# Kernel optimization log

Measured on AMD Instinct MI355X. Metric: run time of the kernel, lower is better.

Reference implementation:

```python
import jax, jax.numpy as jnp
import numpy as np

B, T, QD, KD, E, H, L = 4, 512, 256, 256, 256, 8, 4
DH = E // H
SHAPES = np.array([[64, 64], [32, 32], [16, 16], [8, 8]], dtype=np.int64)
S = int(np.sum(SHAPES[:, 0] * SHAPES[:, 1]))  # 5440


def setup_inputs() -> dict:
    key = jax.random.key(0)
    ks = jax.random.split(key, 16)
    std = 0.02
    return {
        "q": jax.random.normal(ks[0], (B, T, QD), jnp.float32),
        "k": jax.random.normal(ks[1], (B, S, KD), jnp.float32),
        "v": jax.random.normal(ks[2], (B, S, KD), jnp.float32),
        "Wq": jax.random.normal(ks[3], (E, QD), jnp.float32) * std,
        "bq": jnp.zeros((E,), jnp.float32),
        "Wk": jax.random.normal(ks[4], (E, KD), jnp.float32) * std,
        "bk": jnp.zeros((E,), jnp.float32),
        "Wv": jax.random.normal(ks[5], (E, KD), jnp.float32) * std,
        "bv": jnp.zeros((E,), jnp.float32),
        "Wo": jax.random.normal(ks[6], (QD, E), jnp.float32) * std,
        "bo": jnp.zeros((QD,), jnp.float32),
        "Wl": jax.random.normal(ks[7], (H * L, QD), jnp.float32) * std,
        "bl": jnp.zeros((H * L,), jnp.float32),
        "k_spatial_shapes": SHAPES,  # static int metadata (split sizes)
    }


def _heads(x, b):
    # [b, s, E] -> [b, H, s, DH]
    return x.reshape(b, -1, H, DH).transpose(0, 2, 1, 3)


def reference(q, k, v, Wq, bq, Wk, bk, Wv, bv, Wo, bo, Wl, bl, k_spatial_shapes):
    scale = DH ** -0.5
    bsz = q.shape[0]
    # per-head, per-level gate: [B, H, T, L], softmax over levels
    gates = jax.nn.softmax(
        (q @ Wl.T + bl).reshape(bsz, -1, H, L).transpose(0, 2, 1, 3), axis=-1
    )
    qs = _heads((q @ Wq.T + bq) * scale, bsz)   # [B,H,T,DH]
    ks_ = _heads(k @ Wk.T + bk, bsz)            # [B,H,S,DH]
    vs = _heads(v @ Wv.T + bv, bsz)             # [B,H,S,DH]
    scores = jnp.einsum("bhtd,bhsd->bhts", qs, ks_)  # [B,H,T,S]
    sizes = [int(h_ * w_) for h_, w_ in np.asarray(k_spatial_shapes)]
    offs = np.concatenate([[0], np.cumsum(sizes)])
    # segmented softmax per level, weighted by the learned level gate
    pieces = [
        jax.nn.softmax(scores[..., offs[i]:offs[i + 1]], axis=-1) * gates[..., i:i + 1]
        for i in range(len(sizes))
    ]
    attn = jnp.concatenate(pieces, axis=-1)  # [B,H,T,S]
    out = jnp.einsum("bhts,bhsd->bhtd", attn, vs)
    out = out.transpose(0, 2, 1, 3).reshape(bsz, -1, E)
    out = out @ Wo.T + bo
    return out, attn
```

## Files before the change

### kernel.cpp

```cpp
#include <hip/hip_runtime.h>
#include <hip/hip_bf16.h>

#define Bn 4
#define Hn 8
#define Tn 512
#define Sn 5440
#define DHn 32
#define En 256

typedef short bf16x8 __attribute__((ext_vector_type(8)));
typedef float f32x4 __attribute__((ext_vector_type(4)));

static __device__ __forceinline__ unsigned short f2bf(float f) {
    union { float f; unsigned u; } c; c.f = f;
    unsigned r = c.u + 0x7fffu + ((c.u >> 16) & 1u);
    return (unsigned short)(r >> 16);
}

static __device__ __forceinline__ unsigned int cvtpk(float a, float b) {
    __hip_bfloat162 h = __float22bfloat162_rn(make_float2(a, b));
    unsigned int u; __builtin_memcpy(&u, &h, 4); return u;
}

__global__ __launch_bounds__(256) void gates_kernel(
// ... 136 lines not shown
    }
}

__global__ __launch_bounds__(256) void proj_out(
    const float* __restrict__ A, const float* __restrict__ W,
    const float* __restrict__ bias, float* __restrict__ out)
{
    __shared__ unsigned short As[128][40];
    __shared__ unsigned short Ws[128][40];

    int tid = threadIdx.x;
    int l = tid & 63, wid = tid >> 6;
    int wr = wid >> 1, wc = wid & 1;
    int lr = l & 15, lg = l >> 4;
    int row0 = blockIdx.x * 128, col0 = blockIdx.y * 128;

    f32x4 acc[4][4] = {};
    gemm_core(A, W, row0, col0, tid, wr, wc, lr, lg, As, Ws, acc);

    #pragma unroll
    for (int i = 0; i < 4; i++) {
        int m0 = row0 + wr*64 + i*16 + lg*4;
        #pragma unroll
        for (int j = 0; j < 4; j++) {
            int col = col0 + wc*64 + j*16 + lr;
            float bvv = bias[col];
            #pragma unroll
            for (int r = 0; r < 4; r++)
                __builtin_nontemporal_store(acc[i][j][r] + bvv, &out[(size_t)(m0 + r)*256 + col]);
        }
    }
}

__global__ __launch_bounds__(256) void attn_fused(
    const unsigned short* __restrict__ qs, const unsigned short* __restrict__ ks,
    const unsigned short* __restrict__ vt, const float* __restrict__ gates,
    float* __restrict__ attn_out, float* __restrict__ o_tmp)
{
    __shared__ char plds[4][2048];
    __shared__ float lsum[4][4][16];
    __shared__ float denom[4][16];
    __shared__ float outred[4][16][32];

    int n = blockIdx.x;
    int bh = ((n >> 8) << 3) | (n & 7);
    int tt = (n >> 3) & 31;
    int t0 = tt << 4;
    int b = bh >> 3, h = bh & 7;
    int tid = threadIdx.x;
    int l = tid & 63, w = tid >> 6;
    int lr = l & 15, lg = l >> 4;

    bf16x8 aq = *(const bf16x8*)(qs + ((size_t)bh*Tn + t0 + lr)*DHn + lg*8);
    const unsigned short* kb = ks + (size_t)bh * Sn * DHn;
    const unsigned short* vb = vt + (size_t)bh * DHn * Sn;
    const f32x4 fzero = {0.f, 0.f, 0.f, 0.f};

    float lp0 = 0.f, lp1 = 0.f, lp2 = 0.f, lp3 = 0.f;
    bf16x8 kf0, kf1, kf2, kf3;
    {
        const unsigned short* kc_ = kb + (size_t)w * 64 * DHn;
        kf0 = *(const bf16x8*)(kc_ + (size_t)(lr     )*DHn + lg*8);
        kf1 = *(const bf16x8*)(kc_ + (size_t)(16 + lr)*DHn + lg*8);
        kf2 = *(const bf16x8*)(kc_ + (size_t)(32 + lr)*DHn + lg*8);
        kf3 = *(const bf16x8*)(kc_ + (size_t)(48 + lr)*DHn + lg*8);
    }
    for (int c = w; c < 85; c += 4) {
        bf16x8 kn0, kn1, kn2, kn3;
        int cn = c + 4;
        if (cn < 85) {
            const unsigned short* kc_ = kb + (size_t)cn * 64 * DHn;
            kn0 = *(const bf16x8*)(kc_ + (size_t)(lr     )*DHn + lg*8);
            kn1 = *(const bf16x8*)(kc_ + (size_t)(16 + lr)*DHn + lg*8);
            kn2 = *(const bf16x8*)(kc_ + (size_t)(32 + lr)*DHn + lg*8);
            kn3 = *(const bf16x8*)(kc_ + (size_t)(48 + lr)*DHn + lg*8);
        }
        __builtin_amdgcn_s_setprio(1);
        f32x4 s0 = __builtin_amdgcn_mfma_f32_16x16x32_bf16(kf0, aq, fzero, 0, 0, 0);
        f32x4 s1 = __builtin_amdgcn_mfma_f32_16x16x32_bf16(kf1, aq, fzero, 0, 0, 0);
        f32x4 s2 = __builtin_amdgcn_mfma_f32_16x16x32_bf16(kf2, aq, fzero, 0, 0, 0);
        f32x4 s3 = __builtin_amdgcn_mfma_f32_16x16x32_bf16(kf3, aq, fzero, 0, 0, 0);
        __builtin_amdgcn_s_setprio(0);
        float es = exp2f(s0[0]) + exp2f(s0[1]) + exp2f(s0[2]) + exp2f(s0[3])
                 + exp2f(s1[0]) + exp2f(s1[1]) + exp2f(s1[2]) + exp2f(s1[3])
                 + exp2f(s2[0]) + exp2f(s2[1]) + exp2f(s2[2]) + exp2f(s2[3])
                 + exp2f(s3[0]) + exp2f(s3[1]) + exp2f(s3[2]) + exp2f(s3[3]);
        if      (c < 64) lp0 += es;
        else if (c < 80) lp1 += es;
        else if (c < 84) lp2 += es;
        else             lp3 += es;
        kf0 = kn0; kf1 = kn1; kf2 = kn2; kf3 = kn3;
    }
    {
        float v;
        v = lp0; v += __shfl_xor(v, 16); v += __shfl_xor(v, 32); lp0 = v;
        v = lp1; v += __shfl_xor(v, 16); v += __shfl_xor(v, 32); lp1 = v;
        v = lp2; v += __shfl_xor(v, 16); v += __shfl_xor(v, 32); lp2 = v;
        v = lp3; v += __shfl_xor(v, 16); v += __shfl_xor(v, 32); lp3 = v;
    }
    if (l < 16) {
        lsum[w][0][lr] = lp0; lsum[w][1][lr] = lp1;
        lsum[w][2][lr] = lp2; lsum[w][3][lr] = lp3;
    }
    __syncthreads();
    if (tid < 64) {
        int seg = tid >> 4, row = tid & 15;
        denom[seg][row] = lsum[0][seg][row] + lsum[1][seg][row] + lsum[2][seg][row] + lsum[3][seg][row];
    }
    __syncthreads();

    float cf0, cf1, cf2, cf3;
    {
        const float* g = gates + ((size_t)bh*Tn + t0 + lr)*4;
        cf0 = g[0] / denom[0][lr];
        cf1 = g[1] / denom[1][lr];
        cf2 = g[2] / denom[2][lr];
        cf3 = g[3] / denom[3][lr];
    }

    f32x4 acc0 = fzero, acc1 = fzero;
    char* pbase = plds[w];
    float* arow = attn_out + ((size_t)bh*Tn + t0 + lr)*Sn;
    int swz = (lr & 7) << 4;

    bf16x8 vf0, vf1, vf2, vf3;
    {
        const unsigned short* kc_ = kb + (size_t)w * 64 * DHn;
        kf0 = *(const bf16x8*)(kc_ + (size_t)(lr     )*DHn + lg*8);
        kf1 = *(const bf16x8*)(kc_ + (size_t)(16 + lr)*DHn + lg*8);
        kf2 = *(const bf16x8*)(kc_ + (size_t)(32 + lr)*DHn + lg*8);
        kf3 = *(const bf16x8*)(kc_ + (size_t)(48 + lr)*DHn + lg*8);
        vf0 = *(const bf16x8*)(vb + (size_t)(lr     )*Sn + w*64      + lg*8);
        vf1 = *(const bf16x8*)(vb + (size_t)(16 + lr)*Sn + w*64      + lg*8);
        vf2 = *(const bf16x8*)(vb + (size_t)(lr     )*Sn + w*64 + 32 + lg*8);
        vf3 = *(const bf16x8*)(vb + (size_t)(16 + lr)*Sn + w*64 + 32 + lg*8);
    }

    for (int c = w; c < 85; c += 4) {
        bf16x8 kn0, kn1, kn2, kn3, vn0, vn1, vn2, vn3;
        int cn = c + 4;
        if (cn < 85) {
            const unsigned short* kc_ = kb + (size_t)cn * 64 * DHn;
            kn0 = *(const bf16x8*)(kc_ + (size_t)(lr     )*DHn + lg*8);
            kn1 = *(const bf16x8*)(kc_ + (size_t)(16 + lr)*DHn + lg*8);
            kn2 = *(const bf16x8*)(kc_ + (size_t)(32 + lr)*DHn + lg*8);
            kn3 = *(const bf16x8*)(kc_ + (size_t)(48 + lr)*DHn + lg*8);
            vn0 = *(const bf16x8*)(vb + (size_t)(lr     )*Sn + cn*64      + lg*8);
            vn1 = *(const bf16x8*)(vb + (size_t)(16 + lr)*Sn + cn*64      + lg*8);
            vn2 = *(const bf16x8*)(vb + (size_t)(lr     )*Sn + cn*64 + 32 + lg*8);
            vn3 = *(const bf16x8*)(vb + (size_t)(16 + lr)*Sn + cn*64 + 32 + lg*8);
        }
        float cf = (c < 64) ? cf0 : (c < 80) ? cf1 : (c < 84) ? cf2 : cf3;

        __builtin_amdgcn_s_setprio(1);
        f32x4 s0 = __builtin_amdgcn_mfma_f32_16x16x32_bf16(kf0, aq, fzero, 0, 0, 0);
        f32x4 s1 = __builtin_amdgcn_mfma_f32_16x16x32_bf16(kf1, aq, fzero, 0, 0, 0);
        f32x4 s2 = __builtin_amdgcn_mfma_f32_16x16x32_bf16(kf2, aq, fzero, 0, 0, 0);
        f32x4 s3 = __builtin_amdgcn_mfma_f32_16x16x32_bf16(kf3, aq, fzero, 0, 0, 0);
        __builtin_amdgcn_s_setprio(0);

        {
            f32x4 av;
            av[0] = exp2f(s0[0])*cf; av[1] = exp2f(s0[1])*cf; av[2] = exp2f(s0[2])*cf; av[3] = exp2f(s0[3])*cf;
            __builtin_nontemporal_store(av, (f32x4*)(arow + c*64 +   0 + 4*lg));
            uint2 pk; pk.x = cvtpk(av[0], av[1]); pk.y = cvtpk(av[2], av[3]);
            *(uint2*)(pbase + ((lr*128 +   0 + lg*8) ^ swz)) = pk;
            av[0] = exp2f(s1[0])*cf; av[1] = exp2f(s1[1])*cf; av[2] = exp2f(s1[2])*cf; av[3] = exp2f(s1[3])*cf;
            __builtin_nontemporal_store(av, (f32x4*)(arow + c*64 +  16 + 4*lg));
            pk.x = cvtpk(av[0], av[1]); pk.y = cvtpk(av[2], av[3]);
            *(uint2*)(pbase + ((lr*128 +  32 + lg*8) ^ swz)) = pk;
            av[0] = exp2f(s2[0])*cf; av[1] = exp2f(s2[1])*cf; av[2] = exp2f(s2[2])*cf; av[3] = exp2f(s2[3])*cf;
            __builtin_nontemporal_store(av, (f32x4*)(arow + c*64 +  32 + 4*lg));
            pk.x = cvtpk(av[0], av[1]); pk.y = cvtpk(av[2], av[3]);
            *(uint2*)(pbase + ((lr*128 +  64 + lg*8) ^ swz)) = pk;
            av[0] = exp2f(s3[0])*cf; av[1] = exp2f(s3[1])*cf; av[2] = exp2f(s3[2])*cf; av[3] = exp2f(s3[3])*cf;
            __builtin_nontemporal_store(av, (f32x4*)(arow + c*64 +  48 + 4*lg));
            pk.x = cvtpk(av[0], av[1]); pk.y = cvtpk(av[2], av[3]);
            *(uint2*)(pbase + ((lr*128 +  96 + lg*8) ^ swz)) = pk;
        }

        __builtin_amdgcn_s_setprio(1);
        {
            bf16x8 pa0 = *(const bf16x8*)(pbase + ((lr*128 +      lg*16) ^ swz));
            acc0 = __builtin_amdgcn_mfma_f32_16x16x32_bf16(pa0, vf0, acc0, 0, 0, 0);
            acc1 = __builtin_amdgcn_mfma_f32_16x16x32_bf16(pa0, vf1, acc1, 0, 0, 0);
            bf16x8 pa1 = *(const bf16x8*)(pbase + ((lr*128 + 64 + lg*16) ^ swz));
            acc0 = __builtin_amdgcn_mfma_f32_16x16x32_bf16(pa1, vf2, acc0, 0, 0, 0);
            acc1 = __builtin_amdgcn_mfma_f32_16x16x32_bf16(pa1, vf3, acc1, 0, 0, 0);
        }
        __builtin_amdgcn_s_setprio(0);

        kf0 = kn0; kf1 = kn1; kf2 = kn2; kf3 = kn3;
        vf0 = vn0; vf1 = vn1; vf2 = vn2; vf3 = vn3;
    }

    #pragma unroll
    for (int r = 0; r < 4; r++) {
        outred[w][4*lg + r][lr]      = acc0[r];
        outred[w][4*lg + r][16 + lr] = acc1[r];
    }
    __syncthreads();
    #pragma unroll
    for (int i = 0; i < 2; i++) {
        int idx = tid + i*256;
        int row = idx >> 5, d = idx & 31;
        float sum = outred[0][row][d] + outred[1][row][d] + outred[2][row][d] + outred[3][row][d];
        __builtin_nontemporal_store(sum, &o_tmp[((size_t)(b*Tn + t0 + row))*En + h*DHn + d]);
    }
}

extern "C" void kernel_launch(void* const* d_in, const int* in_sizes, int n_in,
                              void* d_out, int out_size, void* d_ws, size_t ws_size,
                              hipStream_t stream)
{
    const float* q  = (const float*)d_in[0];
    const float* k  = (const float*)d_in[1];
    const float* v  = (const float*)d_in[2];
    const float* Wq = (const float*)d_in[3];
    const float* bq = (const float*)d_in[4];
    const float* Wk = (const float*)d_in[5];
    const float* bk = (const float*)d_in[6];
    const float* Wv = (const float*)d_in[7];
    const float* bv = (const float*)d_in[8];
    const float* Wo = (const float*)d_in[9];
    const float* bo = (const float*)d_in[10];
    const float* Wl = (const float*)d_in[11];
    const float* bl = (const float*)d_in[12];

    float* out  = (float*)d_out;
    float* attn = out + (size_t)Bn*Tn*256;

    char* ws = (char*)d_ws;
    unsigned short* qs    = (unsigned short*)ws;
    unsigned short* ksb   = (unsigned short*)(ws + (1u<<20));
    unsigned short* vtb   = (unsigned short*)(ws + (1u<<20) + 11141120u);
    float*          gates = (float*)(ws + (1u<<20) + 2u*11141120u);
    float*          o_tmp = (float*)(ws + (1u<<20) + 2u*11141120u + 262144u);

    gates_kernel<<<Bn*Tn/8, 256, 0, stream>>>(q, Wl, bl, gates);
    proj_kvq<<<dim3((Bn*Sn)/128, 2, 3), 256, 0, stream>>>(
        k, Wk, bk, v, Wv, bv, q, Wq, bq, ksb, vtb, qs);
    attn_fused<<<Bn*Hn*(Tn/16), 256, 0, stream>>>(qs, ksb, vtb, gates, attn, o_tmp);
    proj_out<<<dim3((Bn*Tn)/128, 2), 256, 0, stream>>>(o_tmp, Wo, bo, out);
}
```

Before: 182.7 us.

## Split attention into unnormalized PV pass and separate attn-store kernel

The attention kernel now does one pass over K/V. It accumulates unnormalized exp-weighted V products into four per-level accumulators and applies gate/denominator scaling only at the end, which removes the second QK/PV sweep. Writing the large attn probability matrix moves to a new kernel that recomputes QK scores from the denominators stored in workspace. This trades the duplicated PV work and the serialization of stores behind the reductions for an extra launch, a recomputed QK, and dropped software prefetching. Without max subtraction, keeping unnormalized sums in bf16 P carries some precision risk.

```diff
diff --git a/kernel.cpp b/kernel.cpp
--- a/kernel.cpp
+++ b/kernel.cpp
@@ -192,14 +192,14 @@
     }
 }
 
-__global__ __launch_bounds__(256) void attn_fused(
+__global__ __launch_bounds__(256) void attn_pv(
     const unsigned short* __restrict__ qs, const unsigned short* __restrict__ ks,
     const unsigned short* __restrict__ vt, const float* __restrict__ gates,
-    float* __restrict__ attn_out, float* __restrict__ o_tmp)
+    float* __restrict__ denom_g, float* __restrict__ o_tmp)
 {
     __shared__ char plds[4][2048];
     __shared__ float lsum[4][4][16];
-    __shared__ float denom[4][16];
+    __shared__ float denomS[4][16];
     __shared__ float outred[4][16][32];
 
     int n = blockIdx.x;
@@ -217,40 +217,78 @@
     const f32x4 fzero = {0.f, 0.f, 0.f, 0.f};
 
     float lp0 = 0.f, lp1 = 0.f, lp2 = 0.f, lp3 = 0.f;
-    bf16x8 kf0, kf1, kf2, kf3;
-    {
-        const unsigned short* kc_ = kb + (size_t)w * 64 * DHn;
-        kf0 = *(const bf16x8*)(kc_ + (size_t)(lr     )*DHn + lg*8);
-        kf1 = *(const bf16x8*)(kc_ + (size_t)(16 + lr)*DHn + lg*8);
-        kf2 = *(const bf16x8*)(kc_ + (size_t)(32 + lr)*DHn + lg*8);
-        kf3 = *(const bf16x8*)(kc_ + (size_t)(48 + lr)*DHn + lg*8);
-    }
+    f32x4 A0a = fzero, A0b = fzero, A1a = fzero, A1b = fzero;
+    f32x4 A2a = fzero, A2b = fzero, A3a = fzero, A3b = fzero;
+
+    char* pbase = plds[w];
+    int swz = (lr & 7) << 4;
+
     for (int c = w; c < 85; c += 4) {
-        bf16x8 kn0, kn1, kn2, kn3;
-        int cn = c + 4;
-        if (cn < 85) {
-            const unsigned short* kc_ = kb + (size_t)cn * 64 * DHn;
-            kn0 = *(const bf16x8*)(kc_ + (size_t)(lr     )*DHn + lg*8);
-            kn1 = *(const bf16x8*)(kc_ + (size_t)(16 + lr)*DHn + lg*8);
-            kn2 = *(const bf16x8*)(kc_ + (size_t)(32 + lr)*DHn + lg*8);
-            kn3 = *(const bf16x8*)(kc_ + (size_t)(48 + lr)*DHn + lg*8);
-        }
-        __builtin_amdgcn_s_setprio(1);
+        const unsigned short* kc_ = kb + (size_t)c * 64 * DHn;
+        bf16x8 kf0 = *(const bf16x8*)(kc_ + (size_t)(lr     )*DHn + lg*8);
+        bf16x8 kf1 = *(const bf16x8*)(kc_ + (size_t)(16 + lr)*DHn + lg*8);
+        bf16x8 kf2 = *(const bf16x8*)(kc_ + (size_t)(32 + lr)*DHn + lg*8);
+        bf16x8 kf3 = *(const bf16x8*)(kc_ + (size_t)(48 + lr)*DHn + lg*8);
+
         f32x4 s0 = __builtin_amdgcn_mfma_f32_16x16x32_bf16(kf0, aq, fzero, 0, 0, 0);
         f32x4 s1 = __builtin_amdgcn_mfma_f32_16x16x32_bf16(kf1, aq, fzero, 0, 0, 0);
         f32x4 s2 = __builtin_amdgcn_mfma_f32_16x16x32_bf16(kf2, aq, fzero, 0, 0, 0);
         f32x4 s3 = __builtin_amdgcn_mfma_f32_16x16x32_bf16(kf3, aq, fzero, 0, 0, 0);
-        __builtin_amdgcn_s_setprio(0);
-        float es = exp2f(s0[0]) + exp2f(s0[1]) + exp2f(s0[2]) + exp2f(s0[3])
-                 + exp2f(s1[0]) + exp2f(s1[1]) + exp2f(s1[2]) + exp2f(s1[3])
-                 + exp2f(s2[0]) + exp2f(s2[1]) + exp2f(s2[2]) + exp2f(s2[3])
-                 + exp2f(s3[0]) + exp2f(s3[1]) + exp2f(s3[2]) + exp2f(s3[3]);
-        if      (c < 64) lp0 += es;
-        else if (c < 80) lp1 += es;
-        else if (c < 84) lp2 += es;
-        else             lp3 += es;
-        kf0 = kn0; kf1 = kn1; kf2 = kn2; kf3 = kn3;
-    }
+
+        float es;
+        {
+            float e0 = exp2f(s0[0]), e1 = exp2f(s0[1]), e2 = exp2f(s0[2]), e3 = exp2f(s0[3]);
+            uint2 pk; pk.x = cvtpk(e0, e1); pk.y = cvtpk(e2, e3);
+            *(uint2*)(pbase + ((lr*128 +   0 + lg*8) ^ swz)) = pk;
+            es = e0 + e1 + e2 + e3;
+            e0 = exp2f(s1[0]); e1 = exp2f(s1[1]); e2 = exp2f(s1[2]); e3 = exp2f(s1[3]);
+            pk.x = cvtpk(e0, e1); pk.y = cvtpk(e2, e3);
+            *(uint2*)(pbase + ((lr*128 +  32 + lg*8) ^ swz)) = pk;
+            es += e0 + e1 + e2 + e3;
+            e0 = exp2f(s2[0]); e1 = exp2f(s2[1]); e2 = exp2f(s2[2]); e3 = exp2f(s2[3]);
+            pk.x = cvtpk(e0, e1); pk.y = cvtpk(e2, e3);
+            *(uint2*)(pbase + ((lr*128 +  64 + lg*8) ^ swz)) = pk;
+            es += e0 + e1 + e2 + e3;
+            e0 = exp2f(s3[0]); e1 = exp2f(s3[1]); e2 = exp2f(s3[2]); e3 = exp2f(s3[3]);
+            pk.x = cvtpk(e0, e1); pk.y = cvtpk(e2, e3);
+            *(uint2*)(pbase + ((lr*128 +  96 + lg*8) ^ swz)) = pk;
+            es += e0 + e1 + e2 + e3;
+        }
+
+        bf16x8 vf0 = *(const bf16x8*)(vb + (size_t)(lr     )*Sn + c*64      + lg*8);
+        bf16x8 vf1 = *(const bf16x8*)(vb + (size_t)(16 + lr)*Sn + c*64      + lg*8);
+        bf16x8 vf2 = *(const bf16x8*)(vb + (size_t)(lr     )*Sn + c*64 + 32 + lg*8);
+        bf16x8 vf3 = *(const bf16x8*)(vb + (size_t)(16 + lr)*Sn + c*64 + 32 + lg*8);
+        bf16x8 pa0 = *(const bf16x8*)(pbase + ((lr*128 +      lg*16) ^ swz));
+        bf16x8 pa1 = *(const bf16x8*)(pbase + ((lr*128 + 64 + lg*16) ^ swz));
+
+        if (c < 64) {
+            lp0 += es;
+            A0a = __builtin_amdgcn_mfma_f32_16x16x32_bf16(pa0, vf0, A0a, 0, 0, 0);
+            A0b = __builtin_amdgcn_mfma_f32_16x16x32_bf16(pa0, vf1, A0b, 0, 0, 0);
+            A0a = __builtin_amdgcn_mfma_f32_16x16x32_bf16(pa1, vf2, A0a, 0, 0, 0);
+            A0b = __builtin_amdgcn_mfma_f32_16x16x32_bf16(pa1, vf3, A0b, 0, 0, 0);
+        } else if (c < 80) {
+            lp1 += es;
+            A1a = __builtin_amdgcn_mfma_f32_16x16x32_bf16(pa0, vf0, A1a, 0, 0, 0);
+            A1b = __builtin_amdgcn_mfma_f32_16x16x32_bf16(pa0, vf1, A1b, 0, 0, 0);
+            A1a = __builtin_amdgcn_mfma_f32_16x16x32_bf16(pa1, vf2, A1a, 0, 0, 0);
+            A1b = __builtin_amdgcn_mfma_f32_16x16x32_bf16(pa1, vf3, A1b, 0, 0, 0);
+        } else if (c < 84) {
+            lp2 += es;
+            A2a = __builtin_amdgcn_mfma_f32_16x16x32_bf16(pa0, vf0, A2a, 0, 0, 0);
+            A2b = __builtin_amdgcn_mfma_f32_16x16x32_bf16(pa0, vf1, A2b, 0, 0, 0);
+            A2a = __builtin_amdgcn_mfma_f32_16x16x32_bf16(pa1, vf2, A2a, 0, 0, 0);
+            A2b = __builtin_amdgcn_mfma_f32_16x16x32_bf16(pa1, vf3, A2b, 0, 0, 0);
+        } else {
+            lp3 += es;
+            A3a = __builtin_amdgcn_mfma_f32_16x16x32_bf16(pa0, vf0, A3a, 0, 0, 0);
+            A3b = __builtin_amdgcn_mfma_f32_16x16x32_bf16(pa0, vf1, A3b, 0, 0, 0);
+            A3a = __builtin_amdgcn_mfma_f32_16x16x32_bf16(pa1, vf2, A3a, 0, 0, 0);
+            A3b = __builtin_amdgcn_mfma_f32_16x16x32_bf16(pa1, vf3, A3b, 0, 0, 0);
+        }
+    }
+
     {
         float v;
         v = lp0; v += __shfl_xor(v, 16); v += __shfl_xor(v, 32); lp0 = v;
@@ -265,99 +303,22 @@
     __syncthreads();
     if (tid < 64) {
         int seg = tid >> 4, row = tid & 15;
-        denom[seg][row] = lsum[0][seg][row] + lsum[1][seg][row] + lsum[2][seg][row] + lsum[3][seg][row];
+        float d = lsum[0][seg][row] + lsum[1][seg][row] + lsum[2][seg][row] + lsum[3][seg][row];
+        denomS[seg][row] = d;
+        denom_g[((size_t)bh*Tn + t0 + row)*4 + seg] = d;
     }
     __syncthreads();
-
-    float cf0, cf1, cf2, cf3;
-    {
-        const float* g = gates + ((size_t)bh*Tn + t0 + lr)*4;
-        cf0 = g[0] / denom[0][lr];
-        cf1 = g[1] / denom[1][lr];
-        cf2 = g[2] / denom[2][lr];
-        cf3 = g[3] / denom[3][lr];
-    }
-
-    f32x4 acc0 = fzero, acc1 = fzero;
-    char* pbase = plds[w];
-    float* arow = attn_out + ((size_t)bh*Tn + t0 + lr)*Sn;
-    int swz = (lr & 7) << 4;
-
-    bf16x8 vf0, vf1, vf2, vf3;
-    {
-        const unsigned short* kc_ = kb + (size_t)w * 64 * DHn;
-        kf0 = *(const bf16x8*)(kc_ + (size_t)(lr     )*DHn + lg*8);
-        kf1 = *(const bf16x8*)(kc_ + (size_t)(16 + lr)*DHn + lg*8);
-        kf2 = *(const bf16x8*)(kc_ + (size_t)(32 + lr)*DHn + lg*8);
-        kf3 = *(const bf16x8*)(kc_ + (size_t)(48 + lr)*DHn + lg*8);
-        vf0 = *(const bf16x8*)(vb + (size_t)(lr     )*Sn + w*64      + lg*8);
-        vf1 = *(const bf16x8*)(vb + (size_t)(16 + lr)*Sn + w*64      + lg*8);
-        vf2 = *(const bf16x8*)(vb + (size_t)(lr     )*Sn + w*64 + 32 + lg*8);
-        vf3 = *(const bf16x8*)(vb + (size_t)(16 + lr)*Sn + w*64 + 32 + lg*8);
-    }
-
-    for (int c = w; c < 85; c += 4) {
-        bf16x8 kn0, kn1, kn2, kn3, vn0, vn1, vn2, vn3;
-        int cn = c + 4;
-        if (cn < 85) {
-            const unsigned short* kc_ = kb + (size_t)cn * 64 * DHn;
-            kn0 = *(const bf16x8*)(kc_ + (size_t)(lr     )*DHn + lg*8);
-            kn1 = *(const bf16x8*)(kc_ + (size_t)(16 + lr)*DHn + lg*8);
-            kn2 = *(const bf16x8*)(kc_ + (size_t)(32 + lr)*DHn + lg*8);
-            kn3 = *(const bf16x8*)(kc_ + (size_t)(48 + lr)*DHn + lg*8);
-            vn0 = *(const bf16x8*)(vb + (size_t)(lr     )*Sn + cn*64      + lg*8);
-            vn1 = *(const bf16x8*)(vb + (size_t)(16 + lr)*Sn + cn*64      + lg*8);
-            vn2 = *(const bf16x8*)(vb + (size_t)(lr     )*Sn + cn*64 + 32 + lg*8);
-            vn3 = *(const bf16x8*)(vb + (size_t)(16 + lr)*Sn + cn*64 + 32 + lg*8);
-        }
-        float cf = (c < 64) ? cf0 : (c < 80) ? cf1 : (c < 84) ? cf2 : cf3;
-
-        __builtin_amdgcn_s_setprio(1);
-        f32x4 s0 = __builtin_amdgcn_mfma_f32_16x16x32_bf16(kf0, aq, fzero, 0, 0, 0);
-        f32x4 s1 = __builtin_amdgcn_mfma_f32_16x16x32_bf16(kf1, aq, fzero, 0, 0, 0);
-        f32x4 s2 = __builtin_amdgcn_mfma_f32_16x16x32_bf16(kf2, aq, fzero, 0, 0, 0);
-        f32x4 s3 = __builtin_amdgcn_mfma_f32_16x16x32_bf16(kf3, aq, fzero, 0, 0, 0);
-        __builtin_amdgcn_s_setprio(0);
-
-        {
-            f32x4 av;
-            av[0] = exp2f(s0[0])*cf; av[1] = exp2f(s0[1])*cf; av[2] = exp2f(s0[2])*cf; av[3] = exp2f(s0[3])*cf;
-            __builtin_nontemporal_store(av, (f32x4*)(arow + c*64 +   0 + 4*lg));
-            uint2 pk; pk.x = cvtpk(av[0], av[1]); pk.y = cvtpk(av[2], av[3]);
-            *(uint2*)(pbase + ((lr*128 +   0 + lg*8) ^ swz)) = pk;
-            av[0] = exp2f(s1[0])*cf; av[1] = exp2f(s1[1])*cf; av[2] = exp2f(s1[2])*cf; av[3] = exp2f(s1[3])*cf;
-            __builtin_nontemporal_store(av, (f32x4*)(arow + c*64 +  16 + 4*lg));
-            pk.x = cvtpk(av[0], av[1]); pk.y = cvtpk(av[2], av[3]);
-            *(uint2*)(pbase + ((lr*128 +  32 + lg*8) ^ swz)) = pk;
-            av[0] = exp2f(s2[0])*cf; av[1] = exp2f(s2[1])*cf; av[2] = exp2f(s2[2])*cf; av[3] = exp2f(s2[3])*cf;
-            __builtin_nontemporal_store(av, (f32x4*)(arow + c*64 +  32 + 4*lg));
-            pk.x = cvtpk(av[0], av[1]); pk.y = cvtpk(av[2], av[3]);
-            *(uint2*)(pbase + ((lr*128 +  64 + lg*8) ^ swz)) = pk;
-            av[0] = exp2f(s3[0])*cf; av[1] = exp2f(s3[1])*cf; av[2] = exp2f(s3[2])*cf; av[3] = exp2f(s3[3])*cf;
-            __builtin_nontemporal_store(av, (f32x4*)(arow + c*64 +  48 + 4*lg));
-            pk.x = cvtpk(av[0], av[1]); pk.y = cvtpk(av[2], av[3]);
-            *(uint2*)(pbase + ((lr*128 +  96 + lg*8) ^ swz)) = pk;
-        }
-
-        __builtin_amdgcn_s_setprio(1);
-        {
-            bf16x8 pa0 = *(const bf16x8*)(pbase + ((lr*128 +      lg*16) ^ swz));
-            acc0 = __builtin_amdgcn_mfma_f32_16x16x32_bf16(pa0, vf0, acc0, 0, 0, 0);
-            acc1 = __builtin_amdgcn_mfma_f32_16x16x32_bf16(pa0, vf1, acc1, 0, 0, 0);
-            bf16x8 pa1 = *(const bf16x8*)(pbase + ((lr*128 + 64 + lg*16) ^ swz));
-            acc0 = __builtin_amdgcn_mfma_f32_16x16x32_bf16(pa1, vf2, acc0, 0, 0, 0);
-            acc1 = __builtin_amdgcn_mfma_f32_16x16x32_bf16(pa1, vf3, acc1, 0, 0, 0);
-        }
-        __builtin_amdgcn_s_setprio(0);
-
-        kf0 = kn0; kf1 = kn1; kf2 = kn2; kf3 = kn3;
-        vf0 = vn0; vf1 = vn1; vf2 = vn2; vf3 = vn3;
-    }
 
     #pragma unroll
     for (int r = 0; r < 4; r++) {
-        outred[w][4*lg + r][lr]      = acc0[r];
-        outred[w][4*lg + r][16 + lr] = acc1[r];
+        int row = 4*lg + r;
+        float4 g4 = *(const float4*)(gates + ((size_t)bh*Tn + t0 + row)*4);
+        float c0 = g4.x / denomS[0][row];
+        float c1 = g4.y / denomS[1][row];
+        float c2 = g4.z / denomS[2][row];
+        float c3 = g4.w / denomS[3][row];
+        outred[w][row][lr]      = c0*A0a[r] + c1*A1a[r] + c2*A2a[r] + c3*A3a[r];
+        outred[w][row][16 + lr] = c0*A0b[r] + c1*A1b[r] + c2*A2b[r] + c3*A3b[r];
     }
     __syncthreads();
     #pragma unroll
@@ -366,6 +327,61 @@
         int row = idx >> 5, d = idx & 31;
         float sum = outred[0][row][d] + outred[1][row][d] + outred[2][row][d] + outred[3][row][d];
         __builtin_nontemporal_store(sum, &o_tmp[((size_t)(b*Tn + t0 + row))*En + h*DHn + d]);
+    }
+}
+
+__global__ __launch_bounds__(256) void attn_store(
+    const unsigned short* __restrict__ qs, const unsigned short* __restrict__ ks,
+    const float* __restrict__ gates, const float* __restrict__ denom_g,
+    float* __restrict__ attn_out)
+{
+    int n = blockIdx.x;
+    int bh = ((n >> 8) << 3) | (n & 7);
+    int tt = (n >> 3) & 31;
+    int t0 = tt << 4;
+    int tid = threadIdx.x;
+    int l = tid & 63, w = tid >> 6;
+    int lr = l & 15, lg = l >> 4;
+
+    bf16x8 aq = *(const bf16x8*)(qs + ((size_t)bh*Tn + t0 + lr)*DHn + lg*8);
+    const unsigned short* kb = ks + (size_t)bh * Sn * DHn;
+    const f32x4 fzero = {0.f, 0.f, 0.f, 0.f};
+
+    float cf0, cf1, cf2, cf3;
+    {
+        const float* g  = gates   + ((size_t)bh*Tn + t0 + lr)*4;
+        const float* dn = denom_g + ((size_t)bh*Tn + t0 + lr)*4;
+        cf0 = g[0] / dn[0];
+        cf1 = g[1] / dn[1];
+        cf2 = g[2] / dn[2];
+        cf3 = g[3] / dn[3];
+    }
+
+    float* arow = attn_out + ((size_t)bh*Tn + t0 + lr)*Sn;
+
+    for (int c = w; c < 85; c += 4) {
+        const unsigned short* kc_ = kb + (size_t)c * 64 * DHn;
+        bf16x8 kf0 = *(const bf16x8*)(kc_ + (size_t)(lr     )*DHn + lg*8);
+        bf16x8 kf1 = *(const bf16x8*)(kc_ + (size_t)(16 + lr)*DHn + lg*8);
+        bf16x8 kf2 = *(const bf16x8*)(kc_ + (size_t)(32 + lr)*DHn + lg*8);
+        bf16x8 kf3 = *(const bf16x8*)(kc_ + (size_t)(48 + lr)*DHn + lg*8);
+
+        f32x4 s0 = __builtin_amdgcn_mfma_f32_16x16x32_bf16(kf0, aq, fzero, 0, 0, 0);
+        f32x4 s1 = __builtin_amdgcn_mfma_f32_16x16x32_bf16(kf1, aq, fzero, 0, 0, 0);
+        f32x4 s2 = __builtin_amdgcn_mfma_f32_16x16x32_bf16(kf2, aq, fzero, 0, 0, 0);
+        f32x4 s3 = __builtin_amdgcn_mfma_f32_16x16x32_bf16(kf3, aq, fzero, 0, 0, 0);
+
+        float cf = (c < 64) ? cf0 : (c < 80) ? cf1 : (c < 84) ? cf2 : cf3;
+
+        f32x4 av;
+        av[0] = exp2f(s0[0])*cf; av[1] = exp2f(s0[1])*cf; av[2] = exp2f(s0[2])*cf; av[3] = exp2f(s0[3])*cf;
+        __builtin_nontemporal_store(av, (f32x4*)(arow + c*64 +   0 + 4*lg));
+        av[0] = exp2f(s1[0])*cf; av[1] = exp2f(s1[1])*cf; av[2] = exp2f(s1[2])*cf; av[3] = exp2f(s1[3])*cf;
+        __builtin_nontemporal_store(av, (f32x4*)(arow + c*64 +  16 + 4*lg));
+        av[0] = exp2f(s2[0])*cf; av[1] = exp2f(s2[1])*cf; av[2] = exp2f(s2[2])*cf; av[3] = exp2f(s2[3])*cf;
+        __builtin_nontemporal_store(av, (f32x4*)(arow + c*64 +  32 + 4*lg));
+        av[0] = exp2f(s3[0])*cf; av[1] = exp2f(s3[1])*cf; av[2] = exp2f(s3[2])*cf; av[3] = exp2f(s3[3])*cf;
+        __builtin_nontemporal_store(av, (f32x4*)(arow + c*64 +  48 + 4*lg));
     }
 }
 
@@ -396,10 +412,12 @@
     unsigned short* vtb   = (unsigned short*)(ws + (1u<<20) + 11141120u);
     float*          gates = (float*)(ws + (1u<<20) + 2u*11141120u);
     float*          o_tmp = (float*)(ws + (1u<<20) + 2u*11141120u + 262144u);
+    float*          dnm   = (float*)(ws + (1u<<20) + 2u*11141120u + 262144u + 2097152u);
 
     gates_kernel<<<Bn*Tn/8, 256, 0, stream>>>(q, Wl, bl, gates);
     proj_kvq<<<dim3((Bn*Sn)/128, 2, 3), 256, 0, stream>>>(
         k, Wk, bk, v, Wv, bv, q, Wq, bq, ksb, vtb, qs);
-    attn_fused<<<Bn*Hn*(Tn/16), 256, 0, stream>>>(qs, ksb, vtb, gates, attn, o_tmp);
+    attn_pv<<<Bn*Hn*(Tn/16), 256, 0, stream>>>(qs, ksb, vtb, gates, dnm, o_tmp);
+    attn_store<<<Bn*Hn*(Tn/16), 256, 0, stream>>>(qs, ksb, gates, dnm, attn);
     proj_out<<<dim3((Bn*Tn)/128, 2), 256, 0, stream>>>(o_tmp, Wo, bo, out);
 }
```

After: 258.0 us. 1.41x slower.

## Stage attention probabilities in LDS to coalesce global attn stores

Applied to the files above, without the earlier changes.

Instead of each wave writing its 16x64 fp32 probability tile straight to global memory as scattered 16-byte stores, all four waves now write their chunks into a shared 16x1024-byte staging buffer. After a block barrier, the whole block writes full contiguous 1 KB row segments. The goal is better store coalescing on the large attn output, which likely dominates memory traffic. In exchange the loop is now lockstep across waves, with two __syncthreads per step, 16 KB more LDS per block, and less independent overlap between waves.

```diff
diff --git a/kernel.cpp b/kernel.cpp
--- a/kernel.cpp
+++ b/kernel.cpp
@@ -198,6 +198,7 @@
     float* __restrict__ attn_out, float* __restrict__ o_tmp)
 {
     __shared__ char plds[4][2048];
+    __shared__ char estage[16*1024];
     __shared__ float lsum[4][4][16];
     __shared__ float denom[4][16];
     __shared__ float outred[4][16][32];
@@ -280,7 +281,6 @@
 
     f32x4 acc0 = fzero, acc1 = fzero;
     char* pbase = plds[w];
-    float* arow = attn_out + ((size_t)bh*Tn + t0 + lr)*Sn;
     int swz = (lr & 7) << 4;
 
     bf16x8 vf0, vf1, vf2, vf3;
@@ -296,62 +296,85 @@
         vf3 = *(const bf16x8*)(vb + (size_t)(16 + lr)*Sn + w*64 + 32 + lg*8);
     }
 
-    for (int c = w; c < 85; c += 4) {
-        bf16x8 kn0, kn1, kn2, kn3, vn0, vn1, vn2, vn3;
-        int cn = c + 4;
-        if (cn < 85) {
-            const unsigned short* kc_ = kb + (size_t)cn * 64 * DHn;
-            kn0 = *(const bf16x8*)(kc_ + (size_t)(lr     )*DHn + lg*8);
-            kn1 = *(const bf16x8*)(kc_ + (size_t)(16 + lr)*DHn + lg*8);
-            kn2 = *(const bf16x8*)(kc_ + (size_t)(32 + lr)*DHn + lg*8);
-            kn3 = *(const bf16x8*)(kc_ + (size_t)(48 + lr)*DHn + lg*8);
-            vn0 = *(const bf16x8*)(vb + (size_t)(lr     )*Sn + cn*64      + lg*8);
-            vn1 = *(const bf16x8*)(vb + (size_t)(16 + lr)*Sn + cn*64      + lg*8);
-            vn2 = *(const bf16x8*)(vb + (size_t)(lr     )*Sn + cn*64 + 32 + lg*8);
-            vn3 = *(const bf16x8*)(vb + (size_t)(16 + lr)*Sn + cn*64 + 32 + lg*8);
-        }
-        float cf = (c < 64) ? cf0 : (c < 80) ? cf1 : (c < 84) ? cf2 : cf3;
-
-        __builtin_amdgcn_s_setprio(1);
-        f32x4 s0 = __builtin_amdgcn_mfma_f32_16x16x32_bf16(kf0, aq, fzero, 0, 0, 0);
-        f32x4 s1 = __builtin_amdgcn_mfma_f32_16x16x32_bf16(kf1, aq, fzero, 0, 0, 0);
-        f32x4 s2 = __builtin_amdgcn_mfma_f32_16x16x32_bf16(kf2, aq, fzero, 0, 0, 0);
-        f32x4 s3 = __builtin_amdgcn_mfma_f32_16x16x32_bf16(kf3, aq, fzero, 0, 0, 0);
-        __builtin_amdgcn_s_setprio(0);
-
+    char* ebase = estage + lr*1024;
+    int ecol0 = w*256 + lg*16;
+    int eswz = (lr & 7) << 4;
+
+    for (int step = 0; step < 22; ++step) {
+        int c = step*4 + w;
+        bool act = (c < 85);
+        if (act) {
+            bf16x8 kn0, kn1, kn2, kn3, vn0, vn1, vn2, vn3;
+            int cn = c + 4;
+            if (cn < 85) {
+                const unsigned short* kc_ = kb + (size_t)cn * 64 * DHn;
+                kn0 = *(const bf16x8*)(kc_ + (size_t)(lr     )*DHn + lg*8);
+                kn1 = *(const bf16x8*)(kc_ + (size_t)(16 + lr)*DHn + lg*8);
+                kn2 = *(const bf16x8*)(kc_ + (size_t)(32 + lr)*DHn + lg*8);
+                kn3 = *(const bf16x8*)(kc_ + (size_t)(48 + lr)*DHn + lg*8);
+                vn0 = *(const bf16x8*)(vb + (size_t)(lr     )*Sn + cn*64      + lg*8);
+                vn1 = *(const bf16x8*)(vb + (size_t)(16 + lr)*Sn + cn*64      + lg*8);
+                vn2 = *(const bf16x8*)(vb + (size_t)(lr     )*Sn + cn*64 + 32 + lg*8);
+                vn3 = *(const bf16x8*)(vb + (size_t)(16 + lr)*Sn + cn*64 + 32 + lg*8);
+            }
+            float cf = (c < 64) ? cf0 : (c < 80) ? cf1 : (c < 84) ? cf2 : cf3;
+
+            __builtin_amdgcn_s_setprio(1);
+            f32x4 s0 = __builtin_amdgcn_mfma_f32_16x16x32_bf16(kf0, aq, fzero, 0, 0, 0);
+            f32x4 s1 = __builtin_amdgcn_mfma_f32_16x16x32_bf16(kf1, aq, fzero, 0, 0, 0);
+            f32x4 s2 = __builtin_amdgcn_mfma_f32_16x16x32_bf16(kf2, aq, fzero, 0, 0, 0);
+            f32x4 s3 = __builtin_amdgcn_mfma_f32_16x16x32_bf16(kf3, aq, fzero, 0, 0, 0);
+            __builtin_amdgcn_s_setprio(0);
+
+            {
+                f32x4 av;
+                av[0] = exp2f(s0[0])*cf; av[1] = exp2f(s0[1])*cf; av[2] = exp2f(s0[2])*cf; av[3] = exp2f(s0[3])*cf;
+                *(f32x4*)(ebase + ((ecol0 +   0) ^ eswz)) = av;
+                uint2 pk; pk.x = cvtpk(av[0], av[1]); pk.y = cvtpk(av[2], av[3]);
+                *(uint2*)(pbase + ((lr*128 +   0 + lg*8) ^ swz)) = pk;
+                av[0] = exp2f(s1[0])*cf; av[1] = exp2f(s1[1])*cf; av[2] = exp2f(s1[2])*cf; av[3] = exp2f(s1[3])*cf;
+                *(f32x4*)(ebase + ((ecol0 +  64) ^ eswz)) = av;
+                pk.x = cvtpk(av[0], av[1]); pk.y = cvtpk(av[2], av[3]);
+                *(uint2*)(pbase + ((lr*128 +  32 + lg*8) ^ swz)) = pk;
+                av[0] = exp2f(s2[0])*cf; av[1] = exp2f(s2[1])*cf; av[2] = exp2f(s2[2])*cf; av[3] = exp2f(s2[3])*cf;
+                *(f32x4*)(ebase + ((ecol0 + 128) ^ eswz)) = av;
+                pk.x = cvtpk(av[0], av[1]); pk.y = cvtpk(av[2], av[3]);
+                *(uint2*)(pbase + ((lr*128 +  64 + lg*8) ^ swz)) = pk;
+                av[0] = exp2f(s3[0])*cf; av[1] = exp2f(s3[1])*cf; av[2] = exp2f(s3[2])*cf; av[3] = exp2f(s3[3])*cf;
+                *(f32x4*)(ebase + ((ecol0 + 192) ^ eswz)) = av;
+                pk.x = cvtpk(av[0], av[1]); pk.y = cvtpk(av[2], av[3]);
+                *(uint2*)(pbase + ((lr*128 +  96 + lg*8) ^ swz)) = pk;
+            }
+
+            __builtin_amdgcn_s_setprio(1);
+            {
+                bf16x8 pa0 = *(const bf16x8*)(pbase + ((lr*128 +      lg*16) ^ swz));
+                acc0 = __builtin_amdgcn_mfma_f32_16x16x32_bf16(pa0, vf0, acc0, 0, 0, 0);
+                acc1 = __builtin_amdgcn_mfma_f32_16x16x32_bf16(pa0, vf1, acc1, 0, 0, 0);
+                bf16x8 pa1 = *(const bf16x8*)(pbase + ((lr*128 + 64 + lg*16) ^ swz));
+                acc0 = __builtin_amdgcn_mfma_f32_16x16x32_bf16(pa1, vf2, acc0, 0, 0, 0);
+                acc1 = __builtin_amdgcn_mfma_f32_16x16x32_bf16(pa1, vf3, acc1, 0, 0, 0);
+            }
+            __builtin_amdgcn_s_setprio(0);
+
+            kf0 = kn0; kf1 = kn1; kf2 = kn2; kf3 = kn3;
+            vf0 = vn0; vf1 = vn1; vf2 = vn2; vf3 = vn3;
+        }
+        __syncthreads();
         {
-            f32x4 av;
-            av[0] = exp2f(s0[0])*cf; av[1] = exp2f(s0[1])*cf; av[2] = exp2f(s0[2])*cf; av[3] = exp2f(s0[3])*cf;
-            __builtin_nontemporal_store(av, (f32x4*)(arow + c*64 +   0 + 4*lg));
-            uint2 pk; pk.x = cvtpk(av[0], av[1]); pk.y = cvtpk(av[2], av[3]);
-            *(uint2*)(pbase + ((lr*128 +   0 + lg*8) ^ swz)) = pk;
-            av[0] = exp2f(s1[0])*cf; av[1] = exp2f(s1[1])*cf; av[2] = exp2f(s1[2])*cf; av[3] = exp2f(s1[3])*cf;
-            __builtin_nontemporal_store(av, (f32x4*)(arow + c*64 +  16 + 4*lg));
-            pk.x = cvtpk(av[0], av[1]); pk.y = cvtpk(av[2], av[3]);
-            *(uint2*)(pbase + ((lr*128 +  32 + lg*8) ^ swz)) = pk;
-            av[0] = exp2f(s2[0])*cf; av[1] = exp2f(s2[1])*cf; av[2] = exp2f(s2[2])*cf; av[3] = exp2f(s2[3])*cf;
-            __builtin_nontemporal_store(av, (f32x4*)(arow + c*64 +  32 + 4*lg));
-            pk.x = cvtpk(av[0], av[1]); pk.y = cvtpk(av[2], av[3]);
-            *(uint2*)(pbase + ((lr*128 +  64 + lg*8) ^ swz)) = pk;
-            av[0] = exp2f(s3[0])*cf; av[1] = exp2f(s3[1])*cf; av[2] = exp2f(s3[2])*cf; av[3] = exp2f(s3[3])*cf;
-            __builtin_nontemporal_store(av, (f32x4*)(arow + c*64 +  48 + 4*lg));
-            pk.x = cvtpk(av[0], av[1]); pk.y = cvtpk(av[2], av[3]);
-            *(uint2*)(pbase + ((lr*128 +  96 + lg*8) ^ swz)) = pk;
-        }
-
-        __builtin_amdgcn_s_setprio(1);
-        {
-            bf16x8 pa0 = *(const bf16x8*)(pbase + ((lr*128 +      lg*16) ^ swz));
-            acc0 = __builtin_amdgcn_mfma_f32_16x16x32_bf16(pa0, vf0, acc0, 0, 0, 0);
-            acc1 = __builtin_amdgcn_mfma_f32_16x16x32_bf16(pa0, vf1, acc1, 0, 0, 0);
-            bf16x8 pa1 = *(const bf16x8*)(pbase + ((lr*128 + 64 + lg*16) ^ swz));
-            acc0 = __builtin_amdgcn_mfma_f32_16x16x32_bf16(pa1, vf2, acc0, 0, 0, 0);
-            acc1 = __builtin_amdgcn_mfma_f32_16x16x32_bf16(pa1, vf3, acc1, 0, 0, 0);
-        }
-        __builtin_amdgcn_s_setprio(0);
-
-        kf0 = kn0; kf1 = kn1; kf2 = kn2; kf3 = kn3;
-        vf0 = vn0; vf1 = vn1; vf2 = vn2; vf3 = vn3;
+            int row = tid >> 4, sg = tid & 15;
+            float* ar = attn_out + ((size_t)bh*Tn + t0 + row)*Sn + step*256;
+            int rswz = (row & 7) << 4;
+            #pragma unroll
+            for (int j = 0; j < 4; j++) {
+                int colf = sg*4 + j*64;
+                if (step*256 + colf < Sn) {
+                    f32x4 vv = *(const f32x4*)(estage + row*1024 + ((sg*16 + j*256) ^ rswz));
+                    __builtin_nontemporal_store(vv, (f32x4*)(ar + colf));
+                }
+            }
+        }
+        __syncthreads();
     }
 
     #pragma unroll
```

After: 165.3 us. 9.5% less time.

## Stage attn tiles in LDS to emit full-row coalesced stores

Applied to the files above, without the earlier changes.

In the second pass each wave now handles groups of four consecutive 64-key chunks and stages the fp32 attention values in a per-wave 16KB LDS buffer. It then writes each row as one contiguous 1KB segment instead of scattered 64-byte pieces per lane group. The last chunk is handled separately by wave 3. The first pass drops its register prefetch, and the output reduction reuses the staging buffer. This adds 64KB of LDS per block, which may lower occupancy, and adds extra LDS traffic plus imbalance across waves.

```diff
diff --git a/kernel.cpp b/kernel.cpp
--- a/kernel.cpp
+++ b/kernel.cpp
@@ -197,10 +197,10 @@
     const unsigned short* __restrict__ vt, const float* __restrict__ gates,
     float* __restrict__ attn_out, float* __restrict__ o_tmp)
 {
+    __shared__ char estw[4][16384];
     __shared__ char plds[4][2048];
     __shared__ float lsum[4][4][16];
     __shared__ float denom[4][16];
-    __shared__ float outred[4][16][32];
 
     int n = blockIdx.x;
     int bh = ((n >> 8) << 3) | (n & 7);
@@ -217,24 +217,12 @@
     const f32x4 fzero = {0.f, 0.f, 0.f, 0.f};
 
     float lp0 = 0.f, lp1 = 0.f, lp2 = 0.f, lp3 = 0.f;
-    bf16x8 kf0, kf1, kf2, kf3;
-    {
-        const unsigned short* kc_ = kb + (size_t)w * 64 * DHn;
-        kf0 = *(const bf16x8*)(kc_ + (size_t)(lr     )*DHn + lg*8);
-        kf1 = *(const bf16x8*)(kc_ + (size_t)(16 + lr)*DHn + lg*8);
-        kf2 = *(const bf16x8*)(kc_ + (size_t)(32 + lr)*DHn + lg*8);
-        kf3 = *(const bf16x8*)(kc_ + (size_t)(48 + lr)*DHn + lg*8);
-    }
     for (int c = w; c < 85; c += 4) {
-        bf16x8 kn0, kn1, kn2, kn3;
-        int cn = c + 4;
-        if (cn < 85) {
-            const unsigned short* kc_ = kb + (size_t)cn * 64 * DHn;
-            kn0 = *(const bf16x8*)(kc_ + (size_t)(lr     )*DHn + lg*8);
-            kn1 = *(const bf16x8*)(kc_ + (size_t)(16 + lr)*DHn + lg*8);
-            kn2 = *(const bf16x8*)(kc_ + (size_t)(32 + lr)*DHn + lg*8);
-            kn3 = *(const bf16x8*)(kc_ + (size_t)(48 + lr)*DHn + lg*8);
-        }
+        const unsigned short* kc_ = kb + (size_t)c * 64 * DHn;
+        bf16x8 kf0 = *(const bf16x8*)(kc_ + (size_t)(lr     )*DHn + lg*8);
+        bf16x8 kf1 = *(const bf16x8*)(kc_ + (size_t)(16 + lr)*DHn + lg*8);
+        bf16x8 kf2 = *(const bf16x8*)(kc_ + (size_t)(32 + lr)*DHn + lg*8);
+        bf16x8 kf3 = *(const bf16x8*)(kc_ + (size_t)(48 + lr)*DHn + lg*8);
         __builtin_amdgcn_s_setprio(1);
         f32x4 s0 = __builtin_amdgcn_mfma_f32_16x16x32_bf16(kf0, aq, fzero, 0, 0, 0);
         f32x4 s1 = __builtin_amdgcn_mfma_f32_16x16x32_bf16(kf1, aq, fzero, 0, 0, 0);
@@ -249,7 +237,6 @@
         else if (c < 80) lp1 += es;
         else if (c < 84) lp2 += es;
         else             lp3 += es;
-        kf0 = kn0; kf1 = kn1; kf2 = kn2; kf3 = kn3;
     }
     {
         float v;
@@ -280,66 +267,125 @@
 
     f32x4 acc0 = fzero, acc1 = fzero;
     char* pbase = plds[w];
-    float* arow = attn_out + ((size_t)bh*Tn + t0 + lr)*Sn;
+    char* ebase = estw[w];
     int swz = (lr & 7) << 4;
-
-    bf16x8 vf0, vf1, vf2, vf3;
+    float* abase = attn_out + ((size_t)bh*Tn + t0)*Sn;
+
+    bf16x8 kf0, kf1, kf2, kf3, vf0, vf1, vf2, vf3;
     {
-        const unsigned short* kc_ = kb + (size_t)w * 64 * DHn;
+        int c = w * 4;
+        const unsigned short* kc_ = kb + (size_t)c * 64 * DHn;
         kf0 = *(const bf16x8*)(kc_ + (size_t)(lr     )*DHn + lg*8);
         kf1 = *(const bf16x8*)(kc_ + (size_t)(16 + lr)*DHn + lg*8);
         kf2 = *(const bf16x8*)(kc_ + (size_t)(32 + lr)*DHn + lg*8);
         kf3 = *(const bf16x8*)(kc_ + (size_t)(48 + lr)*DHn + lg*8);
-        vf0 = *(const bf16x8*)(vb + (size_t)(lr     )*Sn + w*64      + lg*8);
-        vf1 = *(const bf16x8*)(vb + (size_t)(16 + lr)*Sn + w*64      + lg*8);
-        vf2 = *(const bf16x8*)(vb + (size_t)(lr     )*Sn + w*64 + 32 + lg*8);
-        vf3 = *(const bf16x8*)(vb + (size_t)(16 + lr)*Sn + w*64 + 32 + lg*8);
-    }
-
-    for (int c = w; c < 85; c += 4) {
-        bf16x8 kn0, kn1, kn2, kn3, vn0, vn1, vn2, vn3;
-        int cn = c + 4;
-        if (cn < 85) {
-            const unsigned short* kc_ = kb + (size_t)cn * 64 * DHn;
-            kn0 = *(const bf16x8*)(kc_ + (size_t)(lr     )*DHn + lg*8);
-            kn1 = *(const bf16x8*)(kc_ + (size_t)(16 + lr)*DHn + lg*8);
-            kn2 = *(const bf16x8*)(kc_ + (size_t)(32 + lr)*DHn + lg*8);
-            kn3 = *(const bf16x8*)(kc_ + (size_t)(48 + lr)*DHn + lg*8);
-            vn0 = *(const bf16x8*)(vb + (size_t)(lr     )*Sn + cn*64      + lg*8);
-            vn1 = *(const bf16x8*)(vb + (size_t)(16 + lr)*Sn + cn*64      + lg*8);
-            vn2 = *(const bf16x8*)(vb + (size_t)(lr     )*Sn + cn*64 + 32 + lg*8);
-            vn3 = *(const bf16x8*)(vb + (size_t)(16 + lr)*Sn + cn*64 + 32 + lg*8);
-        }
-        float cf = (c < 64) ? cf0 : (c < 80) ? cf1 : (c < 84) ? cf2 : cf3;
-
-        __builtin_amdgcn_s_setprio(1);
+        vf0 = *(const bf16x8*)(vb + (size_t)(lr     )*Sn + c*64      + lg*8);
+        vf1 = *(const bf16x8*)(vb + (size_t)(16 + lr)*Sn + c*64      + lg*8);
+        vf2 = *(const bf16x8*)(vb + (size_t)(lr     )*Sn + c*64 + 32 + lg*8);
+        vf3 = *(const bf16x8*)(vb + (size_t)(16 + lr)*Sn + c*64 + 32 + lg*8);
+    }
+
+    for (int g = w; g < 21; g += 4) {
+        float cf = (g < 16) ? cf0 : (g < 20) ? cf1 : cf2;
+        #pragma unroll
+        for (int ct4 = 0; ct4 < 4; ct4++) {
+            int c = g*4 + ct4;
+            __builtin_amdgcn_s_setprio(1);
+            f32x4 s0 = __builtin_amdgcn_mfma_f32_16x16x32_bf16(kf0, aq, fzero, 0, 0, 0);
+            f32x4 s1 = __builtin_amdgcn_mfma_f32_16x16x32_bf16(kf1, aq, fzero, 0, 0, 0);
+            f32x4 s2 = __builtin_amdgcn_mfma_f32_16x16x32_bf16(kf2, aq, fzero, 0, 0, 0);
+            f32x4 s3 = __builtin_amdgcn_mfma_f32_16x16x32_bf16(kf3, aq, fzero, 0, 0, 0);
+            __builtin_amdgcn_s_setprio(0);
+
+            {
+                int e0b = ct4*256;
+                f32x4 av;
+                av[0] = exp2f(s0[0])*cf; av[1] = exp2f(s0[1])*cf; av[2] = exp2f(s0[2])*cf; av[3] = exp2f(s0[3])*cf;
+                *(f32x4*)(ebase + lr*1024 + ((e0b +   0 + lg*16) ^ swz)) = av;
+                uint2 pk; pk.x = cvtpk(av[0], av[1]); pk.y = cvtpk(av[2], av[3]);
+                *(uint2*)(pbase + ((lr*128 +   0 + lg*8) ^ swz)) = pk;
+                av[0] = exp2f(s1[0])*cf; av[1] = exp2f(s1[1])*cf; av[2] = exp2f(s1[2])*cf; av[3] = exp2f(s1[3])*cf;
+                *(f32x4*)(ebase + lr*1024 + ((e0b +  64 + lg*16) ^ swz)) = av;
+                pk.x = cvtpk(av[0], av[1]); pk.y = cvtpk(av[2], av[3]);
+                *(uint2*)(pbase + ((lr*128 +  32 + lg*8) ^ swz)) = pk;
+                av[0] = exp2f(s2[0])*cf; av[1] = exp2f(s2[1])*cf; av[2] = exp2f(s2[2])*cf; av[3] = exp2f(s2[3])*cf;
+                *(f32x4*)(ebase + lr*1024 + ((e0b + 128 + lg*16) ^ swz)) = av;
+                pk.x = cvtpk(av[0], av[1]); pk.y = cvtpk(av[2], av[3]);
+                *(uint2*)(pbase + ((lr*128 +  64 + lg*8) ^ swz)) = pk;
+                av[0] = exp2f(s3[0])*cf; av[1] = exp2f(s3[1])*cf; av[2] = exp2f(s3[2])*cf; av[3] = exp2f(s3[3])*cf;
+                *(f32x4*)(ebase + lr*1024 + ((e0b + 192 + lg*16) ^ swz)) = av;
+                pk.x = cvtpk(av[0], av[1]); pk.y = cvtpk(av[2], av[3]);
+                *(uint2*)(pbase + ((lr*128 +  96 + lg*8) ^ swz)) = pk;
+            }
+
+            __builtin_amdgcn_s_setprio(1);
+            {
+                bf16x8 pa0 = *(const bf16x8*)(pbase + ((lr*128 +      lg*16) ^ swz));
+                acc0 = __builtin_amdgcn_mfma_f32_16x16x32_bf16(pa0, vf0, acc0, 0, 0, 0);
+                acc1 = __builtin_amdgcn_mfma_f32_16x16x32_bf16(pa0, vf1, acc1, 0, 0, 0);
+                bf16x8 pa1 = *(const bf16x8*)(pbase + ((lr*128 + 64 + lg*16) ^ swz));
+                acc0 = __builtin_amdgcn_mfma_f32_16x16x32_bf16(pa1, vf2, acc0, 0, 0, 0);
+                acc1 = __builtin_amdgcn_mfma_f32_16x16x32_bf16(pa1, vf3, acc1, 0, 0, 0);
+            }
+            __builtin_amdgcn_s_setprio(0);
+
+            int cn = (ct4 < 3) ? (c + 1) : ((g + 4) * 4);
+            if (ct4 < 3 || g + 4 < 21) {
+                const unsigned short* kc_ = kb + (size_t)cn * 64 * DHn;
+                kf0 = *(const bf16x8*)(kc_ + (size_t)(lr     )*DHn + lg*8);
+                kf1 = *(const bf16x8*)(kc_ + (size_t)(16 + lr)*DHn + lg*8);
+                kf2 = *(const bf16x8*)(kc_ + (size_t)(32 + lr)*DHn + lg*8);
+                kf3 = *(const bf16x8*)(kc_ + (size_t)(48 + lr)*DHn + lg*8);
+                vf0 = *(const bf16x8*)(vb + (size_t)(lr     )*Sn + cn*64      + lg*8);
+                vf1 = *(const bf16x8*)(vb + (size_t)(16 + lr)*Sn + cn*64      + lg*8);
+                vf2 = *(const bf16x8*)(vb + (size_t)(lr     )*Sn + cn*64 + 32 + lg*8);
+                vf3 = *(const bf16x8*)(vb + (size_t)(16 + lr)*Sn + cn*64 + 32 + lg*8);
+            }
+        }
+        #pragma unroll
+        for (int r = 0; r < 16; r++) {
+            f32x4 vv = *(const f32x4*)(ebase + r*1024 + ((l*16) ^ ((r & 7) << 4)));
+            __builtin_nontemporal_store(vv, (f32x4*)(abase + (size_t)r*Sn + g*256 + l*4));
+        }
+    }
+
+    if (w == 3) {
+        int c = 84;
+        const unsigned short* kc_ = kb + (size_t)c * 64 * DHn;
+        kf0 = *(const bf16x8*)(kc_ + (size_t)(lr     )*DHn + lg*8);
+        kf1 = *(const bf16x8*)(kc_ + (size_t)(16 + lr)*DHn + lg*8);
+        kf2 = *(const bf16x8*)(kc_ + (size_t)(32 + lr)*DHn + lg*8);
+        kf3 = *(const bf16x8*)(kc_ + (size_t)(48 + lr)*DHn + lg*8);
+        vf0 = *(const bf16x8*)(vb + (size_t)(lr     )*Sn + c*64      + lg*8);
+        vf1 = *(const bf16x8*)(vb + (size_t)(16 + lr)*Sn + c*64      + lg*8);
+        vf2 = *(const bf16x8*)(vb + (size_t)(lr     )*Sn + c*64 + 32 + lg*8);
+        vf3 = *(const bf16x8*)(vb + (size_t)(16 + lr)*Sn + c*64 + 32 + lg*8);
+
         f32x4 s0 = __builtin_amdgcn_mfma_f32_16x16x32_bf16(kf0, aq, fzero, 0, 0, 0);
         f32x4 s1 = __builtin_amdgcn_mfma_f32_16x16x32_bf16(kf1, aq, fzero, 0, 0, 0);
         f32x4 s2 = __builtin_amdgcn_mfma_f32_16x16x32_bf16(kf2, aq, fzero, 0, 0, 0);
         f32x4 s3 = __builtin_amdgcn_mfma_f32_16x16x32_bf16(kf3, aq, fzero, 0, 0, 0);
-        __builtin_amdgcn_s_setprio(0);
 
         {
             f32x4 av;
-            av[0] = exp2f(s0[0])*cf; av[1] = exp2f(s0[1])*cf; av[2] = exp2f(s0[2])*cf; av[3] = exp2f(s0[3])*cf;
-            __builtin_nontemporal_store(av, (f32x4*)(arow + c*64 +   0 + 4*lg));
+            av[0] = exp2f(s0[0])*cf3; av[1] = exp2f(s0[1])*cf3; av[2] = exp2f(s0[2])*cf3; av[3] = exp2f(s0[3])*cf3;
+            *(f32x4*)(ebase + lr*1024 + ((  0 + lg*16) ^ swz)) = av;
             uint2 pk; pk.x = cvtpk(av[0], av[1]); pk.y = cvtpk(av[2], av[3]);
             *(uint2*)(pbase + ((lr*128 +   0 + lg*8) ^ swz)) = pk;
-            av[0] = exp2f(s1[0])*cf; av[1] = exp2f(s1[1])*cf; av[2] = exp2f(s1[2])*cf; av[3] = exp2f(s1[3])*cf;
-            __builtin_nontemporal_store(av, (f32x4*)(arow + c*64 +  16 + 4*lg));
+            av[0] = exp2f(s1[0])*cf3; av[1] = exp2f(s1[1])*cf3; av[2] = exp2f(s1[2])*cf3; av[3] = exp2f(s1[3])*cf3;
+            *(f32x4*)(ebase + lr*1024 + (( 64 + lg*16) ^ swz)) = av;
             pk.x = cvtpk(av[0], av[1]); pk.y = cvtpk(av[2], av[3]);
             *(uint2*)(pbase + ((lr*128 +  32 + lg*8) ^ swz)) = pk;
-            av[0] = exp2f(s2[0])*cf; av[1] = exp2f(s2[1])*cf; av[2] = exp2f(s2[2])*cf; av[3] = exp2f(s2[3])*cf;
-            __builtin_nontemporal_store(av, (f32x4*)(arow + c*64 +  32 + 4*lg));
+            av[0] = exp2f(s2[0])*cf3; av[1] = exp2f(s2[1])*cf3; av[2] = exp2f(s2[2])*cf3; av[3] = exp2f(s2[3])*cf3;
+            *(f32x4*)(ebase + lr*1024 + ((128 + lg*16) ^ swz)) = av;
             pk.x = cvtpk(av[0], av[1]); pk.y = cvtpk(av[2], av[3]);
             *(uint2*)(pbase + ((lr*128 +  64 + lg*8) ^ swz)) = pk;
-            av[0] = exp2f(s3[0])*cf; av[1] = exp2f(s3[1])*cf; av[2] = exp2f(s3[2])*cf; av[3] = exp2f(s3[3])*cf;
-            __builtin_nontemporal_store(av, (f32x4*)(arow + c*64 +  48 + 4*lg));
+            av[0] = exp2f(s3[0])*cf3; av[1] = exp2f(s3[1])*cf3; av[2] = exp2f(s3[2])*cf3; av[3] = exp2f(s3[3])*cf3;
+            *(f32x4*)(ebase + lr*1024 + ((192 + lg*16) ^ swz)) = av;
             pk.x = cvtpk(av[0], av[1]); pk.y = cvtpk(av[2], av[3]);
             *(uint2*)(pbase + ((lr*128 +  96 + lg*8) ^ swz)) = pk;
         }
 
-        __builtin_amdgcn_s_setprio(1);
         {
             bf16x8 pa0 = *(const bf16x8*)(pbase + ((lr*128 +      lg*16) ^ swz));
             acc0 = __builtin_amdgcn_mfma_f32_16x16x32_bf16(pa0, vf0, acc0, 0, 0, 0);
@@ -348,23 +394,29 @@
             acc0 = __builtin_amdgcn_mfma_f32_16x16x32_bf16(pa1, vf2, acc0, 0, 0, 0);
             acc1 = __builtin_amdgcn_mfma_f32_16x16x32_bf16(pa1, vf3, acc1, 0, 0, 0);
         }
-        __builtin_amdgcn_s_setprio(0);
-
-        kf0 = kn0; kf1 = kn1; kf2 = kn2; kf3 = kn3;
-        vf0 = vn0; vf1 = vn1; vf2 = vn2; vf3 = vn3;
-    }
-
+
+        #pragma unroll
+        for (int r = 0; r < 16; r++) {
+            if (l < 16) {
+                f32x4 vv = *(const f32x4*)(ebase + r*1024 + ((l*16) ^ ((r & 7) << 4)));
+                __builtin_nontemporal_store(vv, (f32x4*)(abase + (size_t)r*Sn + 5376 + l*4));
+            }
+        }
+    }
+
+    float* ored = (float*)estw[w];
     #pragma unroll
     for (int r = 0; r < 4; r++) {
-        outred[w][4*lg + r][lr]      = acc0[r];
-        outred[w][4*lg + r][16 + lr] = acc1[r];
+        ored[(4*lg + r)*32 + lr]      = acc0[r];
+        ored[(4*lg + r)*32 + 16 + lr] = acc1[r];
     }
     __syncthreads();
     #pragma unroll
     for (int i = 0; i < 2; i++) {
         int idx = tid + i*256;
         int row = idx >> 5, d = idx & 31;
-        float sum = outred[0][row][d] + outred[1][row][d] + outred[2][row][d] + outred[3][row][d];
+        float sum = ((float*)estw[0])[row*32 + d] + ((float*)estw[1])[row*32 + d]
+                  + ((float*)estw[2])[row*32 + d] + ((float*)estw[3])[row*32 + d];
         __builtin_nontemporal_store(sum, &o_tmp[((size_t)(b*Tn + t0 + row))*En + h*DHn + d]);
     }
 }
```

New measurement: 174.2 us. -4.6%, faster.
